# Kernel tuning notes

Measured on AMD Instinct MI355X. Metric: run time of the kernel, lower is better.

The kernel has to match this reference:

```python
import jax, jax.numpy as jnp
import numpy as np
import math

B, S, D_MODEL, H = 4, 256, 2048, 256
HEAD_DIM = D_MODEL // H  # 8


def setup_inputs() -> dict:
    key = jax.random.key(0)
    ks = jax.random.split(key, 10)
    w_scale = 0.02
    inp = {
        "x": jax.random.normal(ks[0], (B, S, D_MODEL), dtype=jnp.float32),
        "phase_shift": jax.random.normal(ks[1], (H, 1, 1), dtype=jnp.float32),
        "Wq": jax.random.normal(ks[2], (D_MODEL, D_MODEL), dtype=jnp.float32) * w_scale,
        "bq": jnp.zeros((D_MODEL,), dtype=jnp.float32),
        "Wk": jax.random.normal(ks[3], (D_MODEL, D_MODEL), dtype=jnp.float32) * w_scale,
        "bk": jnp.zeros((D_MODEL,), dtype=jnp.float32),
        "Wv": jax.random.normal(ks[4], (D_MODEL, D_MODEL), dtype=jnp.float32) * w_scale,
        "bv": jnp.zeros((D_MODEL,), dtype=jnp.float32),
        "Wo": jax.random.normal(ks[5], (D_MODEL, D_MODEL), dtype=jnp.float32) * w_scale,
        "bo": jnp.zeros((D_MODEL,), dtype=jnp.float32),
    }
    return inp


def _forward(x, phase_shift, Wq, bq, Wk, bk, Wv, bv, Wo, bo):
    b, s, dm = x.shape
    h = phase_shift.shape[0]
    d = dm // h
    # projections (torch Linear with random weights; stored as [in,out])
    q = (x @ Wq + bq).reshape(b, s, h, d)
    k = (x @ Wk + bk).reshape(b, s, h, d)
    v = (x @ Wv + bv).reshape(b, s, h, d)
    # complex phase rotation: q *= exp(+i phi), k *= exp(-i phi)
    # phase_shift (h,1,1) broadcasts against (b,s,h,d) -> varies along the s dim (requires s==h)
    c = jnp.cos(phase_shift)  # (h,1,1)
    sn = jnp.sin(phase_shift)
    qr, qi = q * c, q * sn          # Re/Im of rotated q
    kr, ki = k * c, -(k * sn)       # Re/Im of rotated k
    scale = 1.0 / math.sqrt(d)
    # per-(b,s) head-mixing scores: [b,s,h,h], complex matmul split into real/imag
    sr = (jnp.einsum('bshd,bsgd->bshg', qr, kr)
          - jnp.einsum('bshd,bsgd->bshg', qi, ki)) * scale
    si = (jnp.einsum('bshd,bsgd->bshg', qr, ki)
          + jnp.einsum('bshd,bsgd->bshg', qi, kr)) * scale  # analytically 0 (phases cancel)
    attn_r = jax.nn.softmax(sr, axis=-1)
    attn_i = jax.nn.softmax(si, axis=-1)  # faithful dual softmax; v is real so only
    # Re(attention @ v) = attn_r @ v reaches the output (.real is taken before o_proj)
    del attn_i
    out = jnp.einsum('bshg,bsgd->bshd', attn_r, v).reshape(b, s, dm)
    return out @ Wo + bo


def reference(x, phase_shift, Wq, bq, Wk, bk, Wv, bv, Wo, bo):
    return _forward(x, phase_shift, Wq, bq, Wk, bk, Wv, bv, Wo, bo)
```

## Files before the change

### kernel.cpp

```cpp
#include <hip/hip_runtime.h>
#include <math.h>

#define M_TOK 1024
#define DM    2048
#define NH    256
#define HD    8
#define SCALE 0.35355339059327373f

typedef _Float16 f16x8 __attribute__((ext_vector_type(8)));
typedef _Float16 f16x4 __attribute__((ext_vector_type(4)));
typedef float    f32x4 __attribute__((ext_vector_type(4)));

__global__ __launch_bounds__(256) void prep(
    const float* __restrict__ x, _Float16* __restrict__ xh,
    const float* __restrict__ W0, const float* __restrict__ W1,
    const float* __restrict__ W2, const float* __restrict__ W3,
    _Float16* __restrict__ T0, _Float16* __restrict__ T1,
    _Float16* __restrict__ T2, _Float16* __restrict__ T3)
{
    __shared__ float t[64][65];
    const int tid = threadIdx.x;
    const int z   = blockIdx.z;

    if (z == 4) {
        const int i = (blockIdx.y * 32 + blockIdx.x) * 256 + tid;
        const float4 a = ((const float4*)x)[2 * i];
        const float4 b = ((const float4*)x)[2 * i + 1];
        f16x8 v;
        v[0] = (_Float16)a.x; v[1] = (_Float16)a.y; v[2] = (_Float16)a.z; v[3] = (_Float16)a.w;
        v[4] = (_Float16)b.x; v[5] = (_Float16)b.y; v[6] = (_Float16)b.z; v[7] = (_Float16)b.w;
        ((f16x8*)xh)[i] = v;
        return;
    }

    const float* W = (z == 0) ? W0 : (z == 1) ? W1 : (z == 2) ? W2 : W3;
    _Float16*    T = (z == 0) ? T0 : (z == 1) ? T1 : (z == 2) ? T2 : T3;

    const int nb = blockIdx.x * 64;
    const int kb = blockIdx.y * 64;
    const int tr = tid >> 4;
    const int tc = (tid & 15) << 2;

    #pragma unroll
    for (int rr = 0; rr < 4; ++rr) {
        const int k = kb + rr * 16 + tr;
        const float4 v = *(const float4*)&W[(size_t)k * DM + nb + tc];
        t[rr * 16 + tr][tc + 0] = v.x;
        t[rr * 16 + tr][tc + 1] = v.y;
        t[rr * 16 + tr][tc + 2] = v.z;
        t[rr * 16 + tr][tc + 3] = v.w;
    }
    __syncthreads();
    #pragma unroll
    for (int rr = 0; rr < 4; ++rr) {
        const int n = nb + rr * 16 + tr;
        f16x4 v;
        #pragma unroll
        for (int j = 0; j < 4; ++j)
            v[j] = (_Float16)t[tc + j][rr * 16 + tr];
        *(f16x4*)&T[(size_t)n * DM + kb + tc] = v;
    }
}

template<int TI, bool F16OUT>
__global__ __launch_bounds__(512) void gemm_t(
    const _Float16* __restrict__ A,
    const _Float16* __restrict__ Bt0, const float* __restrict__ b0, void* __restrict__ C0,
    const _Float16* __restrict__ Bt1, const float* __restrict__ b1, void* __restrict__ C1,
    const _Float16* __restrict__ Bt2, const float* __restrict__ b2, void* __restrict__ C2)
{
    constexpr int BM = 32 * TI;
    constexpr int NA = 2 * TI;
    constexpr int NB = 8;
    constexpr int NC = NA + NB;
    constexpr int PC = (NC + 7) / 8;

    __shared__ _Float16 As[BM * 32];
    __shared__ _Float16 Bs[128 * 32];

    const int which = blockIdx.x >> 4;
    const int bn    = (blockIdx.x & 15) * 128;
    const int bm    = blockIdx.y * BM;

    const _Float16* Bt   = (which == 0) ? Bt0 : (which == 1) ? Bt1 : Bt2;
    const float*    bias = (which == 0) ? b0  : (which == 1) ? b1  : b2;
    void*           C    = (which == 0) ? C0  : (which == 1) ? C1  : C2;

    const int tid  = threadIdx.x;
    const int lane = tid & 63;
    const int wv   = tid >> 6;
    const int wr   = (wv >> 2) * (16 * TI);
    const int wc   = (wv & 3) * 32;
    const int lr   = lane & 15;
    const int lk   = lane >> 4;

    bool            vld[PC];
    const _Float16* gsrc[PC];
    _Float16*       ldst[PC];
    #pragma unroll
    for (int p = 0; p < PC; ++p) {
        const int c = p * 8 + wv;
        vld[p] = (c < NC);
        if (c < NA) {
            ldst[p] = &As[c * 512];
            gsrc[p] = A + (size_t)(bm + c * 16 + (lane >> 2)) * DM + (lane & 3) * 8;
        } else if (c < NC) {
            ldst[p] = &Bs[(c - NA) * 512];
            gsrc[p] = Bt + (size_t)(bn + (c - NA) * 16 + (lane >> 2)) * DM + (lane & 3) * 8;
        } else {
            ldst[p] = &As[0];
            gsrc[p] = A;
        }
    }

    f32x4 acc[TI][2] = {};

    for (int k0 = 0; k0 < DM; k0 += 32) {
        __syncthreads();
        #pragma unroll
        for (int p = 0; p < PC; ++p) {
            if (vld[p])
                __builtin_amdgcn_global_load_lds(
                    (const __attribute__((address_space(1))) void*)gsrc[p],
                    (__attribute__((address_space(3))) void*)ldst[p], 16, 0, 0);
            gsrc[p] += 32;
        }
        __syncthreads();

        f16x8 aF[TI], bF[2];
        #pragma unroll
        for (int i = 0; i < TI; ++i)
            aF[i] = *(const f16x8*)&As[(wr + i * 16 + lr) * 32 + lk * 8];
        #pragma unroll
        for (int j = 0; j < 2; ++j)
            bF[j] = *(const f16x8*)&Bs[(wc + j * 16 + lr) * 32 + lk * 8];

        #pragma unroll
        for (int i = 0; i < TI; ++i)
            #pragma unroll
            for (int j = 0; j < 2; ++j)
                acc[i][j] = __builtin_amdgcn_mfma_f32_16x16x32_f16(aF[i], bF[j], acc[i][j], 0, 0, 0);
    }

    #pragma unroll
    for (int i = 0; i < TI; ++i) {
        #pragma unroll
        for (int j = 0; j < 2; ++j) {
            const int col = bn + wc + j * 16 + lr;
            const float bv = bias[col];
            #pragma unroll
            for (int r = 0; r < 4; ++r) {
                const int row = bm + wr + i * 16 + lk * 4 + r;
                const float v = acc[i][j][r] + bv;
                if (F16OUT)
                    ((_Float16*)C)[(size_t)row * DM + col] = (_Float16)v;
                else
                    ((float*)C)[(size_t)row * DM + col] = v;
            }
        }
    }
}

__global__ __launch_bounds__(256) void attn_mfma(
    const _Float16* __restrict__ Qh, const _Float16* __restrict__ Kh,
    const _Float16* __restrict__ Vh, _Float16* __restrict__ Oh)
{
    __shared__ _Float16 Vt[8][264];
    __shared__ _Float16 Al[256][72];
    __shared__ _Float16 Ot[256][8];

    const int t    = blockIdx.x;
    const int tid  = threadIdx.x;
    const int lane = tid & 63;
    const int wv   = tid >> 6;
    const int col  = lane & 15;
    const int quad = lane >> 4;
    const int hbase = wv * 64;

    const _Float16* qb = Qh + (size_t)t * DM;
    const _Float16* kb = Kh + (size_t)t * DM;
    const _Float16* vb = Vh + (size_t)t * DM;

    {
        const f16x8 v = *(const f16x8*)(vb + tid * 8);
        #pragma unroll
        for (int d = 0; d < 8; ++d) Vt[d][tid] = v[d];
    }

    f16x8 qf[4];
    #pragma unroll
    for (int ht = 0; ht < 4; ++ht) {
        f16x8 v = {};
        if (quad == 0)
            v = *(const f16x8*)(qb + (hbase + ht * 16 + col) * 8);
        #pragma unroll
        for (int j = 0; j < 8; ++j) qf[ht][j] = v[j] * (_Float16)SCALE;
    }

    __syncthreads();

    const f32x4 zf = {};
    float rsum[4] = {};
    f32x4 oacc[4] = {};

    #pragma unroll 1
    for (int c = 0; c < 4; ++c) {
        const int gchunk = c * 64;

        f16x8 kf[4];
        #pragma unroll
        for (int gt = 0; gt < 4; ++gt) {
            f16x8 v = {};
            if (quad == 0)
                v = *(const f16x8*)(kb + (gchunk + gt * 16 + col) * 8);
            kf[gt] = v;
        }

        f32x4 s[4][4];
        #pragma unroll
        for (int gt = 0; gt < 4; ++gt)
            #pragma unroll
            for (int ht = 0; ht < 4; ++ht)
                s[gt][ht] = __builtin_amdgcn_mfma_f32_16x16x32_f16(kf[gt], qf[ht], zf, 0, 0, 0);

        #pragma unroll
        for (int gt = 0; gt < 4; ++gt) {
            #pragma unroll
            for (int ht = 0; ht < 4; ++ht) {
                f16x4 e4;
                #pragma unroll
                for (int r = 0; r < 4; ++r) {
                    e4[r] = (_Float16)__expf(s[gt][ht][r]);
                    rsum[ht] += (float)e4[r];
                }
                *(f16x4*)&Al[hbase + ht * 16 + col][gt * 16 + quad * 4] = e4;
            }
        }

        #pragma unroll
        for (int ks = 0; ks < 2; ++ks) {
            f16x8 vf = {};
            if (col < 8)
                vf = *(const f16x8*)&Vt[col][gchunk + ks * 32 + quad * 8];
            #pragma unroll
            for (int ht = 0; ht < 4; ++ht) {
                const f16x8 af = *(const f16x8*)&Al[hbase + ht * 16 + col][ks * 32 + quad * 8];
                oacc[ht] = __builtin_amdgcn_mfma_f32_16x16x32_f16(af, vf, oacc[ht], 0, 0, 0);
            }
        }
    }

    #pragma unroll
    for (int ht = 0; ht < 4; ++ht) {
        rsum[ht] += __shfl_xor(rsum[ht], 16, 64);
        rsum[ht] += __shfl_xor(rsum[ht], 32, 64);
    }

    #pragma unroll
    for (int ht = 0; ht < 4; ++ht) {
        #pragma unroll
        for (int r = 0; r < 4; ++r) {
            const float sh = __shfl(rsum[ht], quad * 4 + r, 64);
            const float v  = oacc[ht][r] / sh;
            if (col < 8)
                Ot[hbase + ht * 16 + quad * 4 + r][col] = (_Float16)v;
        }
    }
    const f16x8 ov = *(const f16x8*)&Ot[tid][0];
    *(f16x8*)(Oh + (size_t)t * DM + tid * 8) = ov;
}

extern "C" void kernel_launch(void* const* d_in, const int* in_sizes, int n_in,
                              void* d_out, int out_size, void* d_ws, size_t ws_size,
                              hipStream_t stream)
{
    const float* x  = (const float*)d_in[0];
    const float* Wq = (const float*)d_in[2];
    const float* bq = (const float*)d_in[3];
    const float* Wk = (const float*)d_in[4];
    const float* bk = (const float*)d_in[5];
    const float* Wv = (const float*)d_in[6];
    const float* bv = (const float*)d_in[7];
    const float* Wo = (const float*)d_in[8];
    const float* bo = (const float*)d_in[9];
    float* out = (float*)d_out;

    char* ws = (char*)d_ws;
    _Float16* xh  = (_Float16*)(ws);
    _Float16* Wtq = (_Float16*)(ws + (4u  << 20));
    _Float16* Wtk = (_Float16*)(ws + (12u << 20));
    _Float16* Wtv = (_Float16*)(ws + (20u << 20));
    _Float16* Wto = (_Float16*)(ws + (28u << 20));
    _Float16* Qh  = (_Float16*)(ws + (36u << 20));
    _Float16* Kh  = (_Float16*)(ws + (40u << 20));
    _Float16* Vh  = (_Float16*)(ws + (44u << 20));
    _Float16* Oh  = (_Float16*)(ws + (48u << 20));

    prep<<<dim3(32, 32, 5), dim3(256), 0, stream>>>(
        x, xh, Wq, Wk, Wv, Wo, Wtq, Wtk, Wtv, Wto);

    gemm_t<4, true><<<dim3(48, 8), dim3(512), 0, stream>>>(xh,
        Wtq, bq, (void*)Qh,
        Wtk, bk, (void*)Kh,
        Wtv, bv, (void*)Vh);

    attn_mfma<<<dim3(M_TOK), dim3(256), 0, stream>>>(Qh, Kh, Vh, Oh);

    gemm_t<2, false><<<dim3(16, 16), dim3(512), 0, stream>>>(Oh,
        Wto, bo, (void*)out,
        Wto, bo, (void*)out,
        Wto, bo, (void*)out);
}
```

Before: 222.1 us.

## Double-buffer GEMM LDS tiles with K=64 steps and XOR-swizzled layout

Replaces the single-buffered GEMM with a double-buffered version that prefetches the next K=64 slab into a second LDS buffer while MFMAs run on the current one. LDS rows are XOR-swizzled to cut bank conflicts on fragment reads. The launch changes to 256 threads per block with smaller M tiles, giving a larger grid and launch_bounds(256,3) for occupancy. The trade-off is twice the LDS per block and possibly more register pressure.

```diff
diff --git a/kernel.cpp b/kernel.cpp
--- a/kernel.cpp
+++ b/kernel.cpp
@@ -62,21 +62,24 @@
     }
 }
 
-template<int TI, bool F16OUT>
-__global__ __launch_bounds__(512) void gemm_t(
+template<int WGR, int WGC, int WTR, int WTC, bool F16OUT>
+__global__ __launch_bounds__(256, 3) void gemm_db(
     const _Float16* __restrict__ A,
     const _Float16* __restrict__ Bt0, const float* __restrict__ b0, void* __restrict__ C0,
     const _Float16* __restrict__ Bt1, const float* __restrict__ b1, void* __restrict__ C1,
     const _Float16* __restrict__ Bt2, const float* __restrict__ b2, void* __restrict__ C2)
 {
-    constexpr int BM = 32 * TI;
-    constexpr int NA = 2 * TI;
-    constexpr int NB = 8;
-    constexpr int NC = NA + NB;
-    constexpr int PC = (NC + 7) / 8;
-
-    __shared__ _Float16 As[BM * 32];
-    __shared__ _Float16 Bs[128 * 32];
+    constexpr int BM  = WGR * WTR * 16;
+    constexpr int BN  = WGC * WTC * 16;
+    static_assert(BN == 128, "col tile must be 128");
+    constexpr int NA  = BM / 8;
+    constexpr int NB  = 16;
+    constexpr int NC  = NA + NB;
+    constexpr int CPW = NC / 4;
+    static_assert(NC % 4 == 0);
+    constexpr int BUF = (BM + 128) * 64;
+
+    __shared__ _Float16 smem[2 * BUF];
 
     const int which = blockIdx.x >> 4;
     const int bn    = (blockIdx.x & 15) * 128;
@@ -89,63 +92,88 @@
     const int tid  = threadIdx.x;
     const int lane = tid & 63;
     const int wv   = tid >> 6;
-    const int wr   = (wv >> 2) * (16 * TI);
-    const int wc   = (wv & 3) * 32;
+    const int wr   = (wv / WGC) * (WTR * 16);
+    const int wc   = (wv % WGC) * (WTC * 16);
     const int lr   = lane & 15;
     const int lk   = lane >> 4;
-
-    bool            vld[PC];
-    const _Float16* gsrc[PC];
-    _Float16*       ldst[PC];
-    #pragma unroll
-    for (int p = 0; p < PC; ++p) {
-        const int c = p * 8 + wv;
-        vld[p] = (c < NC);
+    const int rx   = lr & 7;
+
+    const _Float16* gsrc[CPW];
+    int             loff[CPW];
+    #pragma unroll
+    for (int p = 0; p < CPW; ++p) {
+        const int c   = wv * CPW + p;
+        const int kch = ((lane & 7) ^ (lane >> 3)) << 3;
         if (c < NA) {
-            ldst[p] = &As[c * 512];
-            gsrc[p] = A + (size_t)(bm + c * 16 + (lane >> 2)) * DM + (lane & 3) * 8;
-        } else if (c < NC) {
-            ldst[p] = &Bs[(c - NA) * 512];
-            gsrc[p] = Bt + (size_t)(bn + (c - NA) * 16 + (lane >> 2)) * DM + (lane & 3) * 8;
+            const int rl = c * 8 + (lane >> 3);
+            gsrc[p] = A + (size_t)(bm + rl) * DM + kch;
+            loff[p] = c * 512 + lane * 8;
         } else {
-            ldst[p] = &As[0];
-            gsrc[p] = A;
-        }
-    }
-
-    f32x4 acc[TI][2] = {};
-
-    for (int k0 = 0; k0 < DM; k0 += 32) {
+            const int rl = (c - NA) * 8 + (lane >> 3);
+            gsrc[p] = Bt + (size_t)(bn + rl) * DM + kch;
+            loff[p] = BM * 64 + (c - NA) * 512 + lane * 8;
+        }
+    }
+
+    int offA[WTR][2], offB[WTC][2];
+    #pragma unroll
+    for (int ks = 0; ks < 2; ++ks) {
+        const int sw = (((ks << 2) | lk) ^ rx) << 3;
+        #pragma unroll
+        for (int i = 0; i < WTR; ++i)
+            offA[i][ks] = (wr + i * 16 + lr) * 64 + sw;
+        #pragma unroll
+        for (int j = 0; j < WTC; ++j)
+            offB[j][ks] = BM * 64 + (wc + j * 16 + lr) * 64 + sw;
+    }
+
+    f32x4 acc[WTR][WTC] = {};
+
+    auto prefetch = [&](int buf) {
+        #pragma unroll
+        for (int p = 0; p < CPW; ++p) {
+            __builtin_amdgcn_global_load_lds(
+                (const __attribute__((address_space(1))) void*)gsrc[p],
+                (__attribute__((address_space(3))) void*)(smem + buf * BUF + loff[p]),
+                16, 0, 0);
+            gsrc[p] += 64;
+        }
+    };
+
+    auto compute = [&](int buf) {
+        const _Float16* base = smem + buf * BUF;
+        #pragma unroll
+        for (int ks = 0; ks < 2; ++ks) {
+            f16x8 aF[WTR], bF[WTC];
+            #pragma unroll
+            for (int i = 0; i < WTR; ++i)
+                aF[i] = *(const f16x8*)&base[offA[i][ks]];
+            #pragma unroll
+            for (int j = 0; j < WTC; ++j)
+                bF[j] = *(const f16x8*)&base[offB[j][ks]];
+            #pragma unroll
+            for (int i = 0; i < WTR; ++i)
+                #pragma unroll
+                for (int j = 0; j < WTC; ++j)
+                    acc[i][j] = __builtin_amdgcn_mfma_f32_16x16x32_f16(aF[i], bF[j], acc[i][j], 0, 0, 0);
+        }
+    };
+
+    prefetch(0);
+    #pragma unroll 1
+    for (int it2 = 0; it2 < 16; ++it2) {
         __syncthreads();
-        #pragma unroll
-        for (int p = 0; p < PC; ++p) {
-            if (vld[p])
-                __builtin_amdgcn_global_load_lds(
-                    (const __attribute__((address_space(1))) void*)gsrc[p],
-                    (__attribute__((address_space(3))) void*)ldst[p], 16, 0, 0);
-            gsrc[p] += 32;
-        }
+        prefetch(1);
+        compute(0);
         __syncthreads();
-
-        f16x8 aF[TI], bF[2];
-        #pragma unroll
-        for (int i = 0; i < TI; ++i)
-            aF[i] = *(const f16x8*)&As[(wr + i * 16 + lr) * 32 + lk * 8];
-        #pragma unroll
-        for (int j = 0; j < 2; ++j)
-            bF[j] = *(const f16x8*)&Bs[(wc + j * 16 + lr) * 32 + lk * 8];
-
-        #pragma unroll
-        for (int i = 0; i < TI; ++i)
-            #pragma unroll
-            for (int j = 0; j < 2; ++j)
-                acc[i][j] = __builtin_amdgcn_mfma_f32_16x16x32_f16(aF[i], bF[j], acc[i][j], 0, 0, 0);
-    }
-
-    #pragma unroll
-    for (int i = 0; i < TI; ++i) {
-        #pragma unroll
-        for (int j = 0; j < 2; ++j) {
+        if (it2 < 15) prefetch(0);
+        compute(1);
+    }
+
+    #pragma unroll
+    for (int i = 0; i < WTR; ++i) {
+        #pragma unroll
+        for (int j = 0; j < WTC; ++j) {
             const int col = bn + wc + j * 16 + lr;
             const float bv = bias[col];
             #pragma unroll
@@ -299,14 +327,14 @@
     prep<<<dim3(32, 32, 5), dim3(256), 0, stream>>>(
         x, xh, Wq, Wk, Wv, Wo, Wtq, Wtk, Wtv, Wto);
 
-    gemm_t<4, true><<<dim3(48, 8), dim3(512), 0, stream>>>(xh,
+    gemm_db<2, 2, 2, 4, true><<<dim3(48, 16), dim3(256), 0, stream>>>(xh,
         Wtq, bq, (void*)Qh,
         Wtk, bk, (void*)Kh,
         Wtv, bv, (void*)Vh);
 
     attn_mfma<<<dim3(M_TOK), dim3(256), 0, stream>>>(Qh, Kh, Vh, Oh);
 
-    gemm_t<2, false><<<dim3(16, 16), dim3(512), 0, stream>>>(Oh,
+    gemm_db<1, 4, 2, 2, false><<<dim3(16, 32), dim3(256), 0, stream>>>(Oh,
         Wto, bo, (void*)out,
         Wto, bo, (void*)out,
         Wto, bo, (void*)out);
```

New measurement: 201.1 us. 1.1x faster.
